# Kernel optimization log

Measured on AMD Instinct MI355X. Metric: run time of the kernel, lower is better.

## Reference

```python
import jax, jax.numpy as jnp
import numpy as np

B, S, D = 32, 512, 512
H, DK, DV, DFF = 8, 64, 64, 2048
TEMP = float(np.sqrt(DK))  # d_k ** 0.5
COS_EPS = 1e-8             # torch.cosine_similarity eps
LN_EPS = 1e-5


def _layernorm(x, g, b):
    mu = jnp.mean(x, axis=-1, keepdims=True)
    var = jnp.var(x, axis=-1, keepdims=True)
    return (x - mu) * jax.lax.rsqrt(var + LN_EPS) * g + b


def setup_inputs() -> dict:
    key = jax.random.key(0)
    ks = jax.random.split(key, 12)
    s = 0.02
    return {
        "x": jax.random.normal(ks[0], (B, S, D), dtype=jnp.float32),
        "w_q": jax.random.normal(ks[1], (D, H * DK), dtype=jnp.float32) * s,
        "w_k": jax.random.normal(ks[2], (D, H * DK), dtype=jnp.float32) * s,
        "w_v": jax.random.normal(ks[3], (D, H * DV), dtype=jnp.float32) * s,
        "w_o": jax.random.normal(ks[4], (H * DV, D), dtype=jnp.float32) * s,
        "w_ff1": jax.random.normal(ks[5], (D, DFF), dtype=jnp.float32) * s,
        "b_ff1": jnp.zeros((DFF,), dtype=jnp.float32),
        "w_ff2": jax.random.normal(ks[6], (DFF, D), dtype=jnp.float32) * s,
        "b_ff2": jnp.zeros((D,), dtype=jnp.float32),
        "g1": jnp.ones((D,), dtype=jnp.float32),
        "b1": jnp.zeros((D,), dtype=jnp.float32),
        "g2": jnp.ones((D,), dtype=jnp.float32),
        "b2": jnp.zeros((D,), dtype=jnp.float32),
    }


def reference(x, w_q, w_k, w_v, w_o, w_ff1, b_ff1, w_ff2, b_ff2, g1, b1, g2, b2):
    b, s, _ = x.shape
    # projections -> [b, h, s, d]
    q = (x @ w_q).reshape(b, s, H, DK).transpose(0, 2, 1, 3)
    k = (x @ w_k).reshape(b, s, H, DK).transpose(0, 2, 1, 3)
    v = (x @ w_v).reshape(b, s, H, DV).transpose(0, 2, 1, 3)
    # cosine-similarity attention: dot(q,k) / max(||q||*||k||, eps) / temperature
    scores = jnp.einsum("bhqd,bhkd->bhqk", q, k)
    nq = jnp.linalg.norm(q, axis=-1)  # [b,h,s]
    nk = jnp.linalg.norm(k, axis=-1)
    denom = jnp.maximum(nq[:, :, :, None] * nk[:, :, None, :], COS_EPS)
    attn = jax.nn.softmax(scores / denom / TEMP, axis=-1)
    out = jnp.einsum("bhqk,bhkd->bhqd", attn, v)  # [b,h,s,dv]
    out = out.transpose(0, 2, 1, 3).reshape(b, s, H * DV) @ w_o
    # residual + LN1
    h1 = _layernorm(x + out, g1, b1)
    # FFN
    ffn = jax.nn.relu(h1 @ w_ff1 + b_ff1) @ w_ff2 + b_ff2
    # residual + LN2
    return _layernorm(h1 + ffn, g2, b2)
```

## Files before the change

### kernel.cpp

```cpp
#include <hip/hip_runtime.h>
#include <cmath>

typedef __bf16 bf16x8 __attribute__((ext_vector_type(8)));
typedef float  floatx4 __attribute__((ext_vector_type(4)));

#define LN_EPS 1e-5f
#define COS_EPS 1e-8f
#define INV_TEMP 0.125f

static const int Mrows = 16384;

__device__ __forceinline__ void gload_lds16(const void* g, void* l) {
  __builtin_amdgcn_global_load_lds(
      (const __attribute__((address_space(1))) void*)g,
      (__attribute__((address_space(3))) void*)l, 16, 0, 0);
}

__global__ __launch_bounds__(256) void prep_kernel(const float* __restrict__ x, __bf16* __restrict__ xb,
                                                   const float* __restrict__ wq, const float* __restrict__ wk,
                                                   const float* __restrict__ wv, const float* __restrict__ wo,
                                                   const float* __restrict__ wff1, const float* __restrict__ wff2,
                                                   __bf16* __restrict__ tq, __bf16* __restrict__ tk,
                                                   __bf16* __restrict__ tv, __bf16* __restrict__ to_,
                                                   __bf16* __restrict__ tff1, __bf16* __restrict__ tff2) {
  const int bid = blockIdx.x, tid = threadIdx.x;
  if (bid < 8192) {
    int i = bid * 256 + tid;
    float4 v = ((const float4*)x)[i];
    __bf16* d = xb + i * 4;
    d[0] = (__bf16)v.x; d[1] = (__bf16)v.y; d[2] = (__bf16)v.z; d[3] = (__bf16)v.w;
    return;
  }
  __shared__ __bf16 til[64][72];
  int t = bid - 8192;
  const float* src; __bf16* dst; int R, C, bx, by;
  if (t < 256) {
    int w = t >> 6, tt = t & 63;
    const float* srcs[4] = {wq, wk, wv, wo};
    __bf16* dsts[4] = {tq, tk, tv, to_};
    src = srcs[w]; dst = dsts[w]; R = 512; C = 512; bx = tt & 7; by = tt >> 3;
  } else if (t < 512) {
    int tt = t - 256;
    src = wff1; dst = tff1; R = 512; C = 2048; bx = tt & 31; by = tt >> 5;
  } else {
    int tt = t - 512;
    src = wff2; dst = tff2; R = 2048; C = 512; bx = tt & 7; by = tt >> 3;
  }
  const float* s = src + (size_t)(by * 64) * C + bx * 64;
  int r = tid >> 4, c4 = (tid & 15) * 4;
  for (int p = 0; p < 4; ++p) {
    int rr = r + p * 16;
    float4 v = *(const float4*)(s + (size_t)rr * C + c4);
    til[c4 + 0][rr] = (__bf16)v.x;
    til[c4 + 1][rr] = (__bf16)v.y;
    til[c4 + 2][rr] = (__bf16)v.z;
    til[c4 + 3][rr] = (__bf16)v.w;
  }
  __syncthreads();
  __bf16* d = dst + (size_t)(bx * 64) * R + by * 64;
  int orow = tid >> 3, oc8 = (tid & 7) * 8;
  for (int p = 0; p < 2; ++p) {
    int rr = orow + p * 32;
    *(bf16x8*)(d + (size_t)rr * R + oc8) = *(const bf16x8*)(&til[rr][oc8]);
  }
}

template <int EPI>
__global__ __launch_bounds__(256) void gemm_bt(const __bf16* __restrict__ A,
                                               const __bf16* __restrict__ Bt,
                                               void* __restrict__ Cv,
                                               const float* __restrict__ bias,
                                               float* __restrict__ norms,
                                               int nbn, int Ndim, int Kdim) {
  __shared__ __align__(16) __bf16 As[128 * 64];
  __shared__ __align__(16) __bf16 Bs[128 * 64];
  const int tid = threadIdx.x;
  const int wave = tid >> 6, lane = tid & 63;
  const int l15 = lane & 15, quad = lane >> 4;
  const int id = blockIdx.x;
  const int xcd = id & 7, t = id >> 3;
  const int nblk = t % nbn, mblk = (t / nbn) * 8 + xcd;
  const int m0 = mblk * 128, n0 = nblk * 128;
  const int wrow = (wave >> 1) * 64, wcol = (wave & 1) * 64;
  const int rs = lane >> 3;
  const int swz_st = ((lane & 7) ^ rs) * 8;
  const int s7 = l15 & 7;

  floatx4 zero = {0.f, 0.f, 0.f, 0.f};
  floatx4 acc[4][4];
  for (int i = 0; i < 4; ++i)
    for (int j = 0; j < 4; ++j) acc[i][j] = zero;

  for (int kt = 0; kt < Kdim; kt += 64) {
    __syncthreads();
    for (int c = 0; c < 8; ++c) {
      int g = wave * 8 + c;
      const __bf16* src;
      __bf16* dst;
      if (g < 16) {
        int row = m0 + g * 8 + rs;
        src = A + (size_t)row * Kdim + kt + swz_st;
        dst = As + g * 512;
      } else {
        int g2 = g - 16;
        int row = n0 + g2 * 8 + rs;
        src = Bt + (size_t)row * Kdim + kt + swz_st;
        dst = Bs + g2 * 512;
      }
      gload_lds16(src, dst + lane * 8);
    }
    __syncthreads();
    for (int hh = 0; hh < 2; ++hh) {
      int ko = ((hh * 4 + quad) ^ s7) * 8;
      bf16x8 a[4], b[4];
      for (int i = 0; i < 4; ++i)
        a[i] = *(const bf16x8*)(As + (wrow + i * 16 + l15) * 64 + ko);
      for (int j = 0; j < 4; ++j)
        b[j] = *(const bf16x8*)(Bs + (wcol + j * 16 + l15) * 64 + ko);
      for (int i = 0; i < 4; ++i)
        for (int j = 0; j < 4; ++j)
          acc[i][j] = __builtin_amdgcn_mfma_f32_16x16x32_bf16(a[i], b[j], acc[i][j], 0, 0, 0);
    }
  }

  if (EPI == 4) {
    int head_global = (n0 + wcol) >> 6;
    int kind = head_global >> 3;
    if (kind < 2) {
      int h = head_global & 7;
      for (int i = 0; i < 4; ++i)
        for (int r = 0; r < 4; ++r) {
          float sq = 0.f;
          for (int j = 0; j < 4; ++j) {
            float v = acc[i][j][r];
            sq += v * v;
          }
          for (int m = 1; m < 16; m <<= 1) sq += __shfl_xor(sq, m, 64);
          if (l15 == 0) {
            int arow = m0 + wrow + i * 16 + quad * 4 + r;
            int bb = arow >> 9, ss = arow & 511;
            norms[kind * 131072 + ((bb << 3) + h) * 512 + ss] = sqrtf(sq);
          }
        }
    }
  }

  for (int i = 0; i < 4; ++i)
    for (int j = 0; j < 4; ++j) {
      int row = m0 + wrow + i * 16 + quad * 4;
      int col = n0 + wcol + j * 16 + l15;
      float bv = (EPI == 2) ? bias[col] : 0.f;
      for (int r = 0; r < 4; ++r) {
        float v = acc[i][j][r];
        size_t idx = (size_t)(row + r) * Ndim + col;
        if (EPI == 4) {
          ((__bf16*)Cv)[idx] = (__bf16)v;
        } else if (EPI == 1) {
          ((float*)Cv)[idx] = v;
        } else {
          v += bv;
          v = v > 0.f ? v : 0.f;
          ((__bf16*)Cv)[idx] = (__bf16)v;
        }
      }
    }
}

__global__ __launch_bounds__(256) void vtrans_kernel(const __bf16* __restrict__ qkv,
                                                     __bf16* __restrict__ vtg) {
  __shared__ __align__(16) unsigned short til[64][68];
  const int tid = threadIdx.x;
  const int st = blockIdx.x;
  const int bh = blockIdx.y;
  const int b = bh >> 3, h = bh & 7;
  const unsigned short* src = (const unsigned short*)qkv +
      (size_t)(b * 512 + st * 64) * 1536 + 1024 + h * 64;
  for (int it = 0; it < 2; ++it) {
    int row = it * 32 + (tid >> 3);
    int c8 = (tid & 7) * 8;
    bf16x8 v = *(const bf16x8*)((const __bf16*)src + (size_t)row * 1536 + c8);
    for (int i = 0; i < 8; ++i) til[row][c8 + i] = ((unsigned short*)&v)[i];
  }
  __syncthreads();
  unsigned short* dst = (unsigned short*)vtg + (size_t)bh * 32768 + st * 64;
  for (int it = 0; it < 2; ++it) {
    int d = it * 32 + (tid >> 3);
    int s8 = (tid & 7) * 8;
    unsigned short v[8];
    for (int i = 0; i < 8; ++i) v[i] = til[s8 + i][d];
    *(bf16x8*)(dst + (size_t)d * 512 + s8) = *(bf16x8*)v;
  }
}

__global__ __launch_bounds__(256) void attn_kernel(const __bf16* __restrict__ qkv,
                                                   const __bf16* __restrict__ vtg,
                                                   const float* __restrict__ norms,
                                                   __bf16* __restrict__ out) {
  __shared__ __align__(16) __bf16 Ks[64 * 64];
  __shared__ __align__(16) __bf16 Vs[64 * 64];
  __shared__ __align__(16) __bf16 P[4][16 * 72];
  const int tid = threadIdx.x, wave = tid >> 6, lane = tid & 63;
  const int l15 = lane & 15, quad = lane >> 4;
  const int qh = blockIdx.x;
  const int bh = blockIdx.y;
  const int b = bh >> 3, h = bh & 7;
  const int qbase = qh * 256 + wave * 64;
  const int rs = lane >> 3;
  const int swz_st = ((lane & 7) ^ rs) * 8;
  const int s7 = l15 & 7;

  const __bf16* Qb = qkv + (size_t)(b * 512) * 1536 + h * 64;
  const __bf16* Kb = Qb + 512;
  const __bf16* Vtb = vtg + (size_t)bh * 32768;
  const float* nkbase = norms + 131072 + bh * 512;
  __bf16* Pw = P[wave];

  bf16x8 aq[4][2];
  float nq[4][4];
  for (int ch = 0; ch < 4; ++ch) {
    int qrow = qbase + ch * 16;
    aq[ch][0] = *(const bf16x8*)(Qb + (size_t)(qrow + l15) * 1536 + quad * 8);
    aq[ch][1] = *(const bf16x8*)(Qb + (size_t)(qrow + l15) * 1536 + 32 + quad * 8);
    for (int r = 0; r < 4; ++r) nq[ch][r] = norms[bh * 512 + qrow + quad * 4 + r];
  }

  floatx4 zero = {0.f, 0.f, 0.f, 0.f};
  floatx4 o[4][4];
  float lsum[4][4];
  for (int ch = 0; ch < 4; ++ch)
    for (int jd = 0; jd < 4; ++jd) o[ch][jd] = zero;
  for (int ch = 0; ch < 4; ++ch)
    for (int r = 0; r < 4; ++r) lsum[ch][r] = 0.f;

  for (int kt = 0; kt < 8; ++kt) {
    int s0 = kt * 64;
    __syncthreads();
    for (int c = 0; c < 4; ++c) {
      int g = wave * 4 + c;
      const __bf16* src;
      __bf16* dst;
      if (g < 8) {
        int sk = g * 8 + rs;
        src = Kb + (size_t)(s0 + sk) * 1536 + swz_st;
        dst = Ks + g * 512;
      } else {
        int g2 = g - 8;
        int d = g2 * 8 + rs;
        src = Vtb + (size_t)d * 512 + s0 + swz_st;
        dst = Vs + g2 * 512;
      }
      gload_lds16(src, dst + lane * 8);
    }
    __syncthreads();

    float nk[4];
    for (int j = 0; j < 4; ++j) nk[j] = nkbase[s0 + j * 16 + l15];

    for (int ch = 0; ch < 4; ++ch) {
      floatx4 z[4];
      for (int j = 0; j < 4; ++j) {
        int r64 = (j * 16 + l15) * 64;
        bf16x8 b0 = *(const bf16x8*)(Ks + r64 + ((quad ^ s7) * 8));
        bf16x8 b1 = *(const bf16x8*)(Ks + r64 + (((4 + quad) ^ s7) * 8));
        floatx4 zz = zero;
        zz = __builtin_amdgcn_mfma_f32_16x16x32_bf16(aq[ch][0], b0, zz, 0, 0, 0);
        zz = __builtin_amdgcn_mfma_f32_16x16x32_bf16(aq[ch][1], b1, zz, 0, 0, 0);
        z[j] = zz;
      }
      for (int j = 0; j < 4; ++j)
        for (int r = 0; r < 4; ++r) {
          float den = nq[ch][r] * nk[j];
          den = den > COS_EPS ? den : COS_EPS;
          float p = __expf(z[j][r] * __builtin_amdgcn_rcpf(den) * INV_TEMP);
          lsum[ch][r] += p;
          Pw[(quad * 4 + r) * 72 + j * 16 + l15] = (__bf16)p;
        }
      bf16x8 ap0 = *(const bf16x8*)(Pw + l15 * 72 + quad * 8);
      bf16x8 ap1 = *(const bf16x8*)(Pw + l15 * 72 + 32 + quad * 8);
      for (int jd = 0; jd < 4; ++jd) {
        int r64 = (jd * 16 + l15) * 64;
        bf16x8 v0 = *(const bf16x8*)(Vs + r64 + ((quad ^ s7) * 8));
        bf16x8 v1 = *(const bf16x8*)(Vs + r64 + (((4 + quad) ^ s7) * 8));
        o[ch][jd] = __builtin_amdgcn_mfma_f32_16x16x32_bf16(ap0, v0, o[ch][jd], 0, 0, 0);
        o[ch][jd] = __builtin_amdgcn_mfma_f32_16x16x32_bf16(ap1, v1, o[ch][jd], 0, 0, 0);
      }
    }
  }

  for (int ch = 0; ch < 4; ++ch)
    for (int r = 0; r < 4; ++r) {
      float s = lsum[ch][r];
      for (int m = 1; m < 16; m <<= 1) s += __shfl_xor(s, m, 64);
      lsum[ch][r] = __builtin_amdgcn_rcpf(s);
    }
  for (int ch = 0; ch < 4; ++ch)
    for (int jd = 0; jd < 4; ++jd)
      for (int r = 0; r < 4; ++r) {
        int q = qbase + ch * 16 + quad * 4 + r;
        int d = jd * 16 + l15;
        out[(size_t)(b * 512 + q) * 512 + h * 64 + d] = (__bf16)(o[ch][jd][r] * lsum[ch][r]);
      }
}

template <bool X1BF, bool WF, bool WB>
__global__ __launch_bounds__(256) void resid_ln(const float* __restrict__ X1f,
                                                const __bf16* __restrict__ X1b,
                                                const float* __restrict__ X2,
                                                const float* __restrict__ bias,
                                                const float* __restrict__ g,
                                                const float* __restrict__ be,
                                                float* __restrict__ outf,
                                                __bf16* __restrict__ outb) {
  int row = blockIdx.x * 4 + (threadIdx.x >> 6);
  int lane = threadIdx.x & 63;
  float v[8];
  if (X1BF) {
    bf16x8 a = *(const bf16x8*)(X1b + (size_t)row * 512 + lane * 8);
    for (int i = 0; i < 8; ++i) v[i] = (float)a[i];
    const float4* r2 = (const float4*)(X2 + (size_t)row * 512);
    float4 b0 = r2[lane * 2], b1 = r2[lane * 2 + 1];
    v[0] += b0.x; v[1] += b0.y; v[2] += b0.z; v[3] += b0.w;
    v[4] += b1.x; v[5] += b1.y; v[6] += b1.z; v[7] += b1.w;
    if (bias) {
      const float* bp = bias + lane * 8;
      for (int i = 0; i < 8; ++i) v[i] += bp[i];
    }
  } else {
    const float4* r1 = (const float4*)(X1f + (size_t)row * 512);
    const float4* r2 = (const float4*)(X2 + (size_t)row * 512);
    float4 a0 = r1[lane * 2], a1 = r1[lane * 2 + 1];
    float4 b0 = r2[lane * 2], b1 = r2[lane * 2 + 1];
    v[0] = a0.x + b0.x; v[1] = a0.y + b0.y; v[2] = a0.z + b0.z; v[3] = a0.w + b0.w;
    v[4] = a1.x + b1.x; v[5] = a1.y + b1.y; v[6] = a1.z + b1.z; v[7] = a1.w + b1.w;
  }
  float s = 0.f, sq = 0.f;
  for (int i = 0; i < 8; ++i) {
    s += v[i];
    sq += v[i] * v[i];
  }
  for (int m = 1; m < 64; m <<= 1) {
    s += __shfl_xor(s, m, 64);
    sq += __shfl_xor(sq, m, 64);
  }
  float mean = s * (1.f / 512.f);
  float var = sq * (1.f / 512.f) - mean * mean;
  float rstd = rsqrtf(var + LN_EPS);
  const float* gp = g + lane * 8;
  const float* bp2 = be + lane * 8;
  float o[8];
  for (int i = 0; i < 8; ++i) o[i] = (v[i] - mean) * rstd * gp[i] + bp2[i];
  if (WF) {
    float4 w0 = {o[0], o[1], o[2], o[3]}, w1 = {o[4], o[5], o[6], o[7]};
    ((float4*)(outf + (size_t)row * 512))[lane * 2] = w0;
    ((float4*)(outf + (size_t)row * 512))[lane * 2 + 1] = w1;
  }
  if (WB) {
    __bf16 tmp[8];
    for (int i = 0; i < 8; ++i) tmp[i] = (__bf16)o[i];
    *(bf16x8*)(outb + (size_t)row * 512 + lane * 8) = *(bf16x8*)tmp;
  }
}

extern "C" void kernel_launch(void* const* d_in, const int* in_sizes, int n_in,
                              void* d_out, int out_size, void* d_ws, size_t ws_size,
                              hipStream_t stream) {
  const float* x     = (const float*)d_in[0];
  const float* w_q   = (const float*)d_in[1];
  const float* w_k   = (const float*)d_in[2];
  const float* w_v   = (const float*)d_in[3];
  const float* w_o   = (const float*)d_in[4];
  const float* w_ff1 = (const float*)d_in[5];
  const float* b_ff1 = (const float*)d_in[6];
  const float* w_ff2 = (const float*)d_in[7];
  const float* b_ff2 = (const float*)d_in[8];
  const float* g1    = (const float*)d_in[9];
  const float* b1    = (const float*)d_in[10];
  const float* g2    = (const float*)d_in[11];
  const float* b2    = (const float*)d_in[12];
  float* out = (float*)d_out;

  char* ws = (char*)d_ws;
  size_t off = 0;
  auto alloc = [&](size_t bytes) -> void* {
    void* p = ws + off;
    off += (bytes + 255) & ~(size_t)255;
    return p;
  };
  __bf16* xb     = (__bf16*)alloc((size_t)Mrows * 512 * 2);
  __bf16* wt_qkv = (__bf16*)alloc((size_t)1536 * 512 * 2);
  __bf16* wt_o   = (__bf16*)alloc((size_t)512 * 512 * 2);
  __bf16* wt_ff1 = (__bf16*)alloc((size_t)2048 * 512 * 2);
  __bf16* wt_ff2 = (__bf16*)alloc((size_t)512 * 2048 * 2);
  __bf16* qkv    = (__bf16*)alloc((size_t)Mrows * 1536 * 2);
  float*  norms  = (float*)alloc((size_t)262144 * 4);
  __bf16* attn   = (__bf16*)alloc((size_t)Mrows * 512 * 2);
  float*  proj   = (float*)alloc((size_t)Mrows * 512 * 4);
  __bf16* h1b    = (__bf16*)alloc((size_t)Mrows * 512 * 2);
  __bf16* mid    = (__bf16*)alloc((size_t)Mrows * 2048 * 2);
  __bf16* vtg    = mid;

  prep_kernel<<<8960, 256, 0, stream>>>(x, xb, w_q, w_k, w_v, w_o, w_ff1, w_ff2,
                                        wt_qkv, wt_qkv + 512 * 512, wt_qkv + 2 * 512 * 512,
                                        wt_o, wt_ff1, wt_ff2);

  gemm_bt<4><<<dim3(12 * 128), 256, 0, stream>>>(xb, wt_qkv, qkv, nullptr,
                                                 norms, 12, 1536, 512);
  vtrans_kernel<<<dim3(8, 256), 256, 0, stream>>>(qkv, vtg);
  attn_kernel<<<dim3(2, 256), 256, 0, stream>>>(qkv, vtg, norms, attn);
  gemm_bt<1><<<dim3(4 * 128), 256, 0, stream>>>(attn, wt_o, proj, nullptr,
                                                nullptr, 4, 512, 512);
  resid_ln<false, false, true><<<4096, 256, 0, stream>>>(x, nullptr, proj, nullptr,
                                                         g1, b1, nullptr, h1b);
  gemm_bt<2><<<dim3(16 * 128), 256, 0, stream>>>(h1b, wt_ff1, mid, b_ff1,
                                                 nullptr, 16, 2048, 512);
  gemm_bt<1><<<dim3(4 * 128), 256, 0, stream>>>(mid, wt_ff2, proj, nullptr,
                                                nullptr, 4, 512, 2048);
  resid_ln<true, true, false><<<4096, 256, 0, stream>>>(nullptr, h1b, proj, b_ff2,
                                                        g2, b2, out, nullptr);
}
```

Baseline: 349.2 us.

## Stage GEMM epilogue through LDS for coalesced bf16 stores; use bf16 intermediates

The GEMM epilogue now writes its accumulator tile to shared memory and then stores it with 16-byte coalesced vectors, replacing the scattered per-element stores. The output-projection and FF2 results are stored as bf16 instead of fp32, which halves intermediate traffic, and the residual-LN kernel reads them as bf16. The attention grid is flattened so that consecutive blocks cover different heads. The risks are extra rounding of the pre-LayerNorm sums, additional barriers, and a larger shared-memory footprint that may lower occupancy.

Measured after the change: 339.7 us. -2.7%, faster.

```diff
diff --git a/kernel.cpp b/kernel.cpp
--- a/kernel.cpp
+++ b/kernel.cpp
@@ -68,12 +68,13 @@
 template <int EPI>
 __global__ __launch_bounds__(256) void gemm_bt(const __bf16* __restrict__ A,
                                                const __bf16* __restrict__ Bt,
-                                               void* __restrict__ Cv,
+                                               __bf16* __restrict__ Cv,
                                                const float* __restrict__ bias,
                                                float* __restrict__ norms,
                                                int nbn, int Ndim, int Kdim) {
-  __shared__ __align__(16) __bf16 As[128 * 64];
-  __shared__ __align__(16) __bf16 Bs[128 * 64];
+  __shared__ __align__(16) char smem[128 * 144 * 2];
+  __bf16* As = (__bf16*)smem;
+  __bf16* Bs = (__bf16*)(smem + 32768 / 2);
   const int tid = threadIdx.x;
   const int wave = tid >> 6, lane = tid & 63;
   const int l15 = lane & 15, quad = lane >> 4;
@@ -145,25 +146,28 @@
     }
   }
 
+  __syncthreads();
+  __bf16* Cs = (__bf16*)smem;
   for (int i = 0; i < 4; ++i)
     for (int j = 0; j < 4; ++j) {
-      int row = m0 + wrow + i * 16 + quad * 4;
-      int col = n0 + wcol + j * 16 + l15;
-      float bv = (EPI == 2) ? bias[col] : 0.f;
+      int coll = wcol + j * 16 + l15;
+      float bv = (EPI == 2) ? bias[n0 + coll] : 0.f;
       for (int r = 0; r < 4; ++r) {
         float v = acc[i][j][r];
-        size_t idx = (size_t)(row + r) * Ndim + col;
-        if (EPI == 4) {
-          ((__bf16*)Cv)[idx] = (__bf16)v;
-        } else if (EPI == 1) {
-          ((float*)Cv)[idx] = v;
-        } else {
+        if (EPI == 2) {
           v += bv;
           v = v > 0.f ? v : 0.f;
-          ((__bf16*)Cv)[idx] = (__bf16)v;
         }
-      }
-    }
+        Cs[(wrow + i * 16 + quad * 4 + r) * 144 + coll] = (__bf16)v;
+      }
+    }
+  __syncthreads();
+  for (int p = 0; p < 8; ++p) {
+    int row = p * 16 + (tid >> 4);
+    int c8 = (tid & 15) * 8;
+    *(bf16x8*)(Cv + (size_t)(m0 + row) * Ndim + n0 + c8) =
+        *(const bf16x8*)(Cs + row * 144 + c8);
+  }
 }
 
 __global__ __launch_bounds__(256) void vtrans_kernel(const __bf16* __restrict__ qkv,
@@ -201,8 +205,8 @@
   __shared__ __align__(16) __bf16 P[4][16 * 72];
   const int tid = threadIdx.x, wave = tid >> 6, lane = tid & 63;
   const int l15 = lane & 15, quad = lane >> 4;
-  const int qh = blockIdx.x;
-  const int bh = blockIdx.y;
+  const int bh = blockIdx.x & 255;
+  const int qh = blockIdx.x >> 8;
   const int b = bh >> 3, h = bh & 7;
   const int qbase = qh * 256 + wave * 64;
   const int rs = lane >> 3;
@@ -305,7 +309,7 @@
 template <bool X1BF, bool WF, bool WB>
 __global__ __launch_bounds__(256) void resid_ln(const float* __restrict__ X1f,
                                                 const __bf16* __restrict__ X1b,
-                                                const float* __restrict__ X2,
+                                                const __bf16* __restrict__ X2,
                                                 const float* __restrict__ bias,
                                                 const float* __restrict__ g,
                                                 const float* __restrict__ be,
@@ -314,24 +318,20 @@
   int row = blockIdx.x * 4 + (threadIdx.x >> 6);
   int lane = threadIdx.x & 63;
   float v[8];
+  bf16x8 b8 = *(const bf16x8*)(X2 + (size_t)row * 512 + lane * 8);
   if (X1BF) {
     bf16x8 a = *(const bf16x8*)(X1b + (size_t)row * 512 + lane * 8);
-    for (int i = 0; i < 8; ++i) v[i] = (float)a[i];
-    const float4* r2 = (const float4*)(X2 + (size_t)row * 512);
-    float4 b0 = r2[lane * 2], b1 = r2[lane * 2 + 1];
-    v[0] += b0.x; v[1] += b0.y; v[2] += b0.z; v[3] += b0.w;
-    v[4] += b1.x; v[5] += b1.y; v[6] += b1.z; v[7] += b1.w;
-    if (bias) {
-      const float* bp = bias + lane * 8;
-      for (int i = 0; i < 8; ++i) v[i] += bp[i];
-    }
+    for (int i = 0; i < 8; ++i) v[i] = (float)a[i] + (float)b8[i];
   } else {
     const float4* r1 = (const float4*)(X1f + (size_t)row * 512);
-    const float4* r2 = (const float4*)(X2 + (size_t)row * 512);
     float4 a0 = r1[lane * 2], a1 = r1[lane * 2 + 1];
-    float4 b0 = r2[lane * 2], b1 = r2[lane * 2 + 1];
-    v[0] = a0.x + b0.x; v[1] = a0.y + b0.y; v[2] = a0.z + b0.z; v[3] = a0.w + b0.w;
-    v[4] = a1.x + b1.x; v[5] = a1.y + b1.y; v[6] = a1.z + b1.z; v[7] = a1.w + b1.w;
+    v[0] = a0.x; v[1] = a0.y; v[2] = a0.z; v[3] = a0.w;
+    v[4] = a1.x; v[5] = a1.y; v[6] = a1.z; v[7] = a1.w;
+    for (int i = 0; i < 8; ++i) v[i] += (float)b8[i];
+  }
+  if (bias) {
+    const float* bp = bias + lane * 8;
+    for (int i = 0; i < 8; ++i) v[i] += bp[i];
   }
   float s = 0.f, sq = 0.f;
   for (int i = 0; i < 8; ++i) {
@@ -394,10 +394,11 @@
   __bf16* qkv    = (__bf16*)alloc((size_t)Mrows * 1536 * 2);
   float*  norms  = (float*)alloc((size_t)262144 * 4);
   __bf16* attn   = (__bf16*)alloc((size_t)Mrows * 512 * 2);
-  float*  proj   = (float*)alloc((size_t)Mrows * 512 * 4);
+  __bf16* projb  = (__bf16*)alloc((size_t)Mrows * 512 * 2);
   __bf16* h1b    = (__bf16*)alloc((size_t)Mrows * 512 * 2);
   __bf16* mid    = (__bf16*)alloc((size_t)Mrows * 2048 * 2);
   __bf16* vtg    = mid;
+  __bf16* f2o    = attn;
 
   prep_kernel<<<8960, 256, 0, stream>>>(x, xb, w_q, w_k, w_v, w_o, w_ff1, w_ff2,
                                         wt_qkv, wt_qkv + 512 * 512, wt_qkv + 2 * 512 * 512,
@@ -406,15 +407,15 @@
   gemm_bt<4><<<dim3(12 * 128), 256, 0, stream>>>(xb, wt_qkv, qkv, nullptr,
                                                  norms, 12, 1536, 512);
   vtrans_kernel<<<dim3(8, 256), 256, 0, stream>>>(qkv, vtg);
-  attn_kernel<<<dim3(2, 256), 256, 0, stream>>>(qkv, vtg, norms, attn);
-  gemm_bt<1><<<dim3(4 * 128), 256, 0, stream>>>(attn, wt_o, proj, nullptr,
+  attn_kernel<<<dim3(512), 256, 0, stream>>>(qkv, vtg, norms, attn);
+  gemm_bt<0><<<dim3(4 * 128), 256, 0, stream>>>(attn, wt_o, projb, nullptr,
                                                 nullptr, 4, 512, 512);
-  resid_ln<false, false, true><<<4096, 256, 0, stream>>>(x, nullptr, proj, nullptr,
+  resid_ln<false, false, true><<<4096, 256, 0, stream>>>(x, nullptr, projb, nullptr,
                                                          g1, b1, nullptr, h1b);
   gemm_bt<2><<<dim3(16 * 128), 256, 0, stream>>>(h1b, wt_ff1, mid, b_ff1,
                                                  nullptr, 16, 2048, 512);
-  gemm_bt<1><<<dim3(4 * 128), 256, 0, stream>>>(mid, wt_ff2, proj, nullptr,
+  gemm_bt<0><<<dim3(4 * 128), 256, 0, stream>>>(mid, wt_ff2, f2o, nullptr,
                                                 nullptr, 4, 512, 2048);
-  resid_ln<true, true, false><<<4096, 256, 0, stream>>>(nullptr, h1b, proj, b_ff2,
+  resid_ln<true, true, false><<<4096, 256, 0, stream>>>(nullptr, h1b, f2o, b_ff2,
                                                         g2, b2, out, nullptr);
 }
```
